# Performance work log

Measured on AMD Instinct MI355X. Metric: run time of the kernel, lower is better.

The kernel has to match this reference:

```python
import jax, jax.numpy as jnp
import numpy as np
from jax import lax

EPS = 1e-6
RADIUS = (5, 5, 5)          # box-filter window (must be odd for shape consistency)
GRADIENT_TYPE = "symmetric"  # {'active','passive','symmetric'}
SHAPE = (1, 1, 256, 256, 256)


def _box1d(x, axis, k):
    """Running-sum (integral image) 1D box filter of width k, 'same' padding floor(k/2)."""
    pad = (k - 1) // 2
    cfg = [(0, 0)] * x.ndim
    cfg[axis] = (pad, pad)
    xp = jnp.pad(x, cfg)
    c = jnp.cumsum(xp, axis=axis)
    cfg2 = [(0, 0)] * x.ndim
    cfg2[axis] = (1, 0)
    c = jnp.pad(c, cfg2)
    n = c.shape[axis]
    return lax.slice_in_dim(c, k, n, axis=axis) - lax.slice_in_dim(c, 0, n - k, axis=axis)


def _box3d(x):
    # separable uniform (all-ones) 3D box filter == F.conv3d with ones kernel
    for ax, k in zip((2, 3, 4), RADIUS):
        x = _box1d(x, ax, k)
    return x


def _grad1d(x, axis):
    """torch.gradient: central differences inside, one-sided at the edges, spacing=1."""
    n = x.shape[axis]
    central = (lax.slice_in_dim(x, 2, n, axis=axis) - lax.slice_in_dim(x, 0, n - 2, axis=axis)) * 0.5
    first = lax.slice_in_dim(x, 1, 2, axis=axis) - lax.slice_in_dim(x, 0, 1, axis=axis)
    last = lax.slice_in_dim(x, n - 1, n, axis=axis) - lax.slice_in_dim(x, n - 2, n - 1, axis=axis)
    return jnp.concatenate([first, central, last], axis=axis)


def _ncc_forces(image, reference_image):
    npix = float(np.prod(RADIUS))
    sum_i = _box3d(image)
    sum_r = _box3d(reference_image)
    sum_ii = _box3d(image * image)
    sum_rr = _box3d(reference_image * reference_image)
    sum_ir = _box3d(image * reference_image)

    image_mean = sum_i / npix
    reference_image_mean = sum_i / npix  # NOTE: faithful to original (uses sum_i, not sum_r)

    var_r = sum_rr - 2.0 * reference_image_mean * sum_r + npix * reference_image_mean * reference_image_mean
    var_i = sum_ii - 2.0 * image_mean * sum_i + npix * image_mean * image_mean
    cross = (sum_ir - reference_image_mean * sum_i - image_mean * sum_r
             + npix * image_mean * reference_image_mean)

    if GRADIENT_TYPE == "active":
        grads = [_grad1d(image, a) for a in (2, 3, 4)]
    elif GRADIENT_TYPE == "passive":
        grads = [_grad1d(reference_image, a) for a in (2, 3, 4)]
    elif GRADIENT_TYPE == "symmetric":
        grads = [0.5 * (_grad1d(image, a) + _grad1d(reference_image, a)) for a in (2, 3, 4)]
    else:
        raise ValueError("Unknown gradient type")

    factor = 2.0 * cross / (var_i * var_r + EPS) * (image - cross / var_r * reference_image)
    return -factor * jnp.concatenate(grads, axis=1)  # (B, 3, D, H, W)


def setup_inputs() -> dict:
    key = jax.random.key(0)
    k1, k2 = jax.random.split(key)
    return {
        "image": jax.random.normal(k1, SHAPE, dtype=jnp.float32),
        "mask": jnp.ones(SHAPE, dtype=jnp.float32),
        "reference_image": jax.random.normal(k2, SHAPE, dtype=jnp.float32),
        "reference_mask": jnp.ones(SHAPE, dtype=jnp.float32),
    }


def reference(image, mask, reference_image, reference_mask):
    # mask / reference_mask are accepted but unused, exactly as in the original module.
    return _ncc_forces(image, reference_image)
```

## Files before the change

### kernel.cpp

```cpp
#include <hip/hip_runtime.h>


#define DIM 256
#define TX  32
#define TY  8
#define ZCH 32
#define PXA 41
#define PY  12
#define NT  256
#define RS  5
#define YW  40
#define NF  5

#define LDS_BAR() asm volatile("s_waitcnt lgkmcnt(0)\n\ts_barrier" ::: "memory")

#define STEP(K, I, ISSUE, COMMIT) do {                                         \
    constexpr int sZ   = ((K) + 3) % RS;                                       \
    constexpr int sZP  = ((K) + 4) % RS;                                       \
    constexpr int sZM1 = ((K) + 2) % RS;                                       \
    constexpr int sZM2 = ((K) + 1) % RS;                                       \
    const int i_ = (I);                                                        \
         \
    if (pfAct) {                                                               \
        if (COMMIT) {                                                          \
            float* d_ = praw + (sZP * PY + prow) * PXA + pcol;                 \
            d_[0] = pf.x; d_[1] = pf.y; d_[2] = pf.z; d_[3] = pf.w;            \
        }                                                                      \
        if (ISSUE) {                                                           \
            float4 v_ = make_float4(0.f, 0.f, 0.f, 0.f);                       \
            if ((z0 + i_) < DIM && pxyOk)                                      \
                v_ = *(const float4*)pcur;                                     \
            pcur += (size_t)(DIM * DIM);                                       \
            pf = v_;                                                           \
        }                                                                      \
    }                                                                          \
    const int b_ = i_ & 1;                                                     \
            \
    if (bAct) {                                                                \
        float sA0=0.f,sA1=0.f,sB0=0.f,sB1=0.f,sAA0=0.f,sAA1=0.f;               \
        float sBB0=0.f,sBB1=0.f,sAB0=0.f,sAB1=0.f;                             \
        _Pragma("unroll")                                                      \
        for (int dy = 0; dy < 5; ++dy) {                                       \
            const float aI0 = rawI[sZ][brow + dy][bcol];                       \
            const float aI1 = rawI[sZ][brow + dy][bcol + 1];                   \
            const float aR0 = rawR[sZ][brow + dy][bcol];                       \
            const float aR1 = rawR[sZ][brow + dy][bcol + 1];                   \
            sA0 += aI0; sA1 += aI1; sB0 += aR0; sB1 += aR1;                    \
            sAA0 = fmaf(aI0, aI0, sAA0); sAA1 = fmaf(aI1, aI1, sAA1);          \
            sBB0 = fmaf(aR0, aR0, sBB0); sBB1 = fmaf(aR1, aR1, sBB1);          \
            sAB0 = fmaf(aI0, aR0, sAB0); sAB1 = fmaf(aI1, aR1, sAB1);          \
        }                                                                      \
        float* yp_ = &ytmp[b_][brow][bcol][0];                                 \
        yp_[0] = sA0; yp_[1] = sB0; yp_[2] = sAA0; yp_[3] = sBB0;              \
        yp_[4] = sAB0;                                                         \
        yp_[5] = sA1; yp_[6] = sB1; yp_[7] = sAA1; yp_[8] = sBB1;              \
        yp_[9] = sAB1;                                                         \
    }                                                                          \
    LDS_BAR();                                                                 \
         \
    float n_[NF];                                                              \
    {                                                                          \
        const float* yb_ = &ytmp[b_][ty][tx + 2][0];                           \
        _Pragma("unroll")                                                      \
        for (int f = 0; f < NF; ++f)                                           \
            n_[f] = yb_[f] + yb_[f+5] + yb_[f+10] + yb_[f+15] + yb_[f+20];     \
    }                                                                          \
                                 \
    cIm = cI0; cI0 = cIp; cIp = rawI[sZM1][ly][lx];                            \
    cRm = cR0; cR0 = cRp; cRp = rawR[sZM1][ly][lx];                            \
                                        \
    if (i_ >= 4) {                                                             \
        const int zc = z0 - 4 + i_;                                            \
        float zs[NF];                                                          \
        _Pragma("unroll")                                                      \
        for (int f = 0; f < NF; ++f)                                           \
            zs[f] = H[((K)+1)%RS][f] + H[((K)+2)%RS][f] + H[((K)+3)%RS][f]     \
                  + H[((K)+4)%RS][f] + n_[f];                                  \
        const float m     = zs[0] * (1.0f / 125.0f);                           \
        const float var_r = zs[3] - 2.0f * m * zs[1] + 125.0f * m * m;         \
        const float var_i = zs[2] - 2.0f * m * zs[0] + 125.0f * m * m;         \
        const float cross = zs[4] - m * zs[0] - m * zs[1] + 125.0f * m * m;    \
        float giz, grz;                                                        \
        if (zc == 0)            { giz = cIp - cI0; grz = cRp - cR0; }          \
        else if (zc == DIM - 1) { giz = cI0 - cIm; grz = cR0 - cRm; }          \
        else { giz = 0.5f * (cIp - cIm); grz = 0.5f * (cRp - cRm); }           \
        const float iyp = rawI[sZM2][ly + 1][lx], iym = rawI[sZM2][ly - 1][lx];\
        const float ryp = rawR[sZM2][ly + 1][lx], rym = rawR[sZM2][ly - 1][lx];\
        const float ixp = rawI[sZM2][ly][lx + 1], ixm = rawI[sZM2][ly][lx - 1];\
        const float rxp = rawR[sZM2][ly][lx + 1], rxm = rawR[sZM2][ly][lx - 1];\
        float giy, gry;                                                        \
        if (gy == 0)            { giy = iyp - cI0; gry = ryp - cR0; }          \
        else if (gy == DIM - 1) { giy = cI0 - iym; gry = cR0 - rym; }          \
        else { giy = 0.5f * (iyp - iym); gry = 0.5f * (ryp - rym); }           \
        float gix, grx;                                                        \
        if (gx == 0)            { gix = ixp - cI0; grx = rxp - cR0; }          \
        else if (gx == DIM - 1) { gix = cI0 - ixm; grx = cR0 - rxm; }          \
        else { gix = 0.5f * (ixp - ixm); grx = 0.5f * (rxp - rxm); }           \
        const float inv_d = __builtin_amdgcn_rcpf(fmaf(var_i, var_r, 1e-6f));  \
        const float inv_r = __builtin_amdgcn_rcpf(var_r);                      \
        const float factor = 2.0f * cross * inv_d * (cI0 - cross * inv_r * cR0);\
        const size_t CS    = (size_t)DIM * DIM * DIM;                          \
        const size_t base_ = ((size_t)zc * DIM + gy) * DIM + gx;               \
        __builtin_nontemporal_store(-factor * 0.5f * (giz + grz),              \
                                    &gOut[base_]);                             \
        __builtin_nontemporal_store(-factor * 0.5f * (giy + gry),              \
                                    &gOut[base_ + CS]);                        \
        __builtin_nontemporal_store(-factor * 0.5f * (gix + grx),              \
                                    &gOut[base_ + 2 * CS]);                    \
    }                                                                          \
                                 \
    _Pragma("unroll")                                                          \
    for (int f = 0; f < NF; ++f) H[(K)][f] = n_[f];                            \
} while (0)

__global__ __launch_bounds__(NT, 5) void ncc_forces_kernel(
    const float* __restrict__ gI,
    const float* __restrict__ gR,
    float* __restrict__ gOut)
{
    __shared__ float rawI[RS][PY][PXA];
    __shared__ float rawR[RS][PY][PXA];
    __shared__ float ytmp[2][TY][YW][NF];

    const int t  = threadIdx.x;
    const int tx = t & 31;
    const int ty = t >> 5;
    const int x0 = blockIdx.x * TX;
    const int y0 = blockIdx.y * TY;
    const int z0 = blockIdx.z * ZCH;

    const bool pfI   = (t < 120);
    const bool pfR   = (t >= 128 && t < 248);
    const bool pfAct = pfI || pfR;
    const int  pid   = pfI ? t : (t - 128);
    const int  prow  = pid / 10;
    const int  pcol  = (pid - prow * 10) * 4;
    const int  pgy   = y0 - 2 + prow;
    const int  pgx   = x0 - 4 + pcol;
    const float* pbase = pfI ? gI : gR;
    float*       praw  = pfI ? &rawI[0][0][0] : &rawR[0][0][0];
    const bool   pxyOk = ((unsigned)pgy < DIM) && ((unsigned)pgx < DIM);
    const size_t pgoff = pxyOk ? ((size_t)pgy * DIM + pgx) : 0;

    const bool bAct = (t < 144);
    const int  brow = t / 18;
    const int  bcol = 2 + (t - brow * 18) * 2;

    const int gy = y0 + ty;
    const int gx = x0 + tx;
    const int ly = ty + 2, lx = tx + 4;

    float4 pf = make_float4(0.f, 0.f, 0.f, 0.f);
    const float* pcur = pbase + (size_t)z0 * (DIM * DIM) + pgoff;

    float H[RS][NF];
    #pragma unroll
    for (int a = 0; a < RS; ++a)
        #pragma unroll
        for (int f = 0; f < NF; ++f) H[a][f] = 0.f;
    float cIm = 0.f, cI0 = 0.f, cIp = 0.f, cRm = 0.f, cR0 = 0.f, cRp = 0.f;

    if (pfAct) {
        float4 v = make_float4(0.f, 0.f, 0.f, 0.f);
        if ((z0 - 2) >= 0 && pxyOk)
            v = *(const float4*)(pbase + (size_t)(z0 - 2) * (DIM * DIM) + pgoff);
        float* d0 = praw + (3 * PY + prow) * PXA + pcol;
        d0[0] = v.x; d0[1] = v.y; d0[2] = v.z; d0[3] = v.w;
        float4 w = make_float4(0.f, 0.f, 0.f, 0.f);
        if ((z0 - 1) >= 0 && pxyOk)
            w = *(const float4*)(pbase + (size_t)(z0 - 1) * (DIM * DIM) + pgoff);
        pf = w;
    }
    LDS_BAR();

    #pragma clang loop unroll(disable)
    for (int ii = 0; ii < 30; ii += 5) {
        STEP(0, ii + 0, true, true);
        STEP(1, ii + 1, true, true);
        STEP(2, ii + 2, true, true);
        STEP(3, ii + 3, true, true);
        STEP(4, ii + 4, true, true);
    }
    STEP(0, 30, true,  true);
    STEP(1, 31, true,  true);
    STEP(2, 32, true,  true);
    STEP(3, 33, true,  true);
    STEP(4, 34, false, true);
    STEP(0, 35, false, false);
}

extern "C" void kernel_launch(void* const* d_in, const int* in_sizes, int n_in,
                              void* d_out, int out_size, void* d_ws, size_t ws_size,
                              hipStream_t stream) {
    const float* img = (const float*)d_in[0];
    const float* ref = (const float*)d_in[2];
    float* out = (float*)d_out;

    dim3 grid(DIM / TX, DIM / TY, DIM / ZCH);
    ncc_forces_kernel<<<grid, NT, 0, stream>>>(img, ref, out);
}
```

Before: 397.5 us.

## Interleave image and reference in shared memory as float2 for vector LDS access

Stores the image and reference tiles together in one interleaved float2 shared array instead of two separate float arrays. The box-filter x-pass can then read both values for two columns with a single float4 LDS load, and the gradient and center reads become float2 loads. Prefetch threads now load float2 from both inputs and commit a single float4 per step. Occupancy hint drops from 5 to 4 blocks, and LDS bank-conflict behaviour changes with the new 42-wide padded stride.

```diff
diff --git a/kernel.cpp b/kernel.cpp
--- a/kernel.cpp
+++ b/kernel.cpp
@@ -1,16 +1,16 @@
 #include <hip/hip_runtime.h>
 
 
-#define DIM 256
-#define TX  32
-#define TY  8
-#define ZCH 32
-#define PXA 41
-#define PY  12
-#define NT  256
-#define RS  5
-#define YW  40
-#define NF  5
+#define DIM  256
+#define TX   32
+#define TY   8
+#define ZCH  32
+#define PXA2 42
+#define PY   12
+#define NT   256
+#define RS   5
+#define YW   40
+#define NF   5
 
 #define LDS_BAR() asm volatile("s_waitcnt lgkmcnt(0)\n\ts_barrier" ::: "memory")
 
@@ -23,32 +23,33 @@
          \
     if (pfAct) {                                                               \
         if (COMMIT) {                                                          \
-            float* d_ = praw + (sZP * PY + prow) * PXA + pcol;                 \
-            d_[0] = pf.x; d_[1] = pf.y; d_[2] = pf.z; d_[3] = pf.w;            \
+            *(float4*)&rawIR[sZP][prow][pcell] =                               \
+                make_float4(pfi.x, pfr.x, pfi.y, pfr.y);                       \
         }                                                                      \
         if (ISSUE) {                                                           \
-            float4 v_ = make_float4(0.f, 0.f, 0.f, 0.f);                       \
-            if ((z0 + i_) < DIM && pxyOk)                                      \
-                v_ = *(const float4*)pcur;                                     \
-            pcur += (size_t)(DIM * DIM);                                       \
-            pf = v_;                                                           \
+            float2 vi = make_float2(0.f, 0.f), vr = make_float2(0.f, 0.f);     \
+            if ((z0 + i_) < DIM && pxyOk) {                                    \
+                vi = *(const float2*)pcurI;                                    \
+                vr = *(const float2*)pcurR;                                    \
+            }                                                                  \
+            pcurI += (size_t)(DIM * DIM);                                      \
+            pcurR += (size_t)(DIM * DIM);                                      \
+            pfi = vi; pfr = vr;                                                \
         }                                                                      \
     }                                                                          \
     const int b_ = i_ & 1;                                                     \
-            \
+        \
     if (bAct) {                                                                \
         float sA0=0.f,sA1=0.f,sB0=0.f,sB1=0.f,sAA0=0.f,sAA1=0.f;               \
         float sBB0=0.f,sBB1=0.f,sAB0=0.f,sAB1=0.f;                             \
         _Pragma("unroll")                                                      \
         for (int dy = 0; dy < 5; ++dy) {                                       \
-            const float aI0 = rawI[sZ][brow + dy][bcol];                       \
-            const float aI1 = rawI[sZ][brow + dy][bcol + 1];                   \
-            const float aR0 = rawR[sZ][brow + dy][bcol];                       \
-            const float aR1 = rawR[sZ][brow + dy][bcol + 1];                   \
-            sA0 += aI0; sA1 += aI1; sB0 += aR0; sB1 += aR1;                    \
-            sAA0 = fmaf(aI0, aI0, sAA0); sAA1 = fmaf(aI1, aI1, sAA1);          \
-            sBB0 = fmaf(aR0, aR0, sBB0); sBB1 = fmaf(aR1, aR1, sBB1);          \
-            sAB0 = fmaf(aI0, aR0, sAB0); sAB1 = fmaf(aI1, aR1, sAB1);          \
+            const float4 v = *(const float4*)&rawIR[sZ][brow + dy][bcol];      \
+            sA0 += v.x; sB0 += v.y; sA1 += v.z; sB1 += v.w;                    \
+            sAA0 = fmaf(v.x, v.x, sAA0); sBB0 = fmaf(v.y, v.y, sBB0);          \
+            sAB0 = fmaf(v.x, v.y, sAB0);                                       \
+            sAA1 = fmaf(v.z, v.z, sAA1); sBB1 = fmaf(v.w, v.w, sBB1);          \
+            sAB1 = fmaf(v.z, v.w, sAB1);                                       \
         }                                                                      \
         float* yp_ = &ytmp[b_][brow][bcol][0];                                 \
         yp_[0] = sA0; yp_[1] = sB0; yp_[2] = sAA0; yp_[3] = sBB0;              \
@@ -65,9 +66,12 @@
         for (int f = 0; f < NF; ++f)                                           \
             n_[f] = yb_[f] + yb_[f+5] + yb_[f+10] + yb_[f+15] + yb_[f+20];     \
     }                                                                          \
-                                 \
-    cIm = cI0; cI0 = cIp; cIp = rawI[sZM1][ly][lx];                            \
-    cRm = cR0; cR0 = cRp; cRp = rawR[sZM1][ly][lx];                            \
+                       \
+    {                                                                          \
+        const float2 c_ = rawIR[sZM1][ly][lx];                                 \
+        cIm = cI0; cI0 = cIp; cIp = c_.x;                                      \
+        cRm = cR0; cR0 = cRp; cRp = c_.y;                                      \
+    }                                                                          \
                                         \
     if (i_ >= 4) {                                                             \
         const int zc = z0 - 4 + i_;                                            \
@@ -84,18 +88,18 @@
         if (zc == 0)            { giz = cIp - cI0; grz = cRp - cR0; }          \
         else if (zc == DIM - 1) { giz = cI0 - cIm; grz = cR0 - cRm; }          \
         else { giz = 0.5f * (cIp - cIm); grz = 0.5f * (cRp - cRm); }           \
-        const float iyp = rawI[sZM2][ly + 1][lx], iym = rawI[sZM2][ly - 1][lx];\
-        const float ryp = rawR[sZM2][ly + 1][lx], rym = rawR[sZM2][ly - 1][lx];\
-        const float ixp = rawI[sZM2][ly][lx + 1], ixm = rawI[sZM2][ly][lx - 1];\
-        const float rxp = rawR[sZM2][ly][lx + 1], rxm = rawR[sZM2][ly][lx - 1];\
+        const float2 cyp = rawIR[sZM2][ly + 1][lx];                            \
+        const float2 cym = rawIR[sZM2][ly - 1][lx];                            \
+        const float2 cxp = rawIR[sZM2][ly][lx + 1];                            \
+        const float2 cxm = rawIR[sZM2][ly][lx - 1];                            \
         float giy, gry;                                                        \
-        if (gy == 0)            { giy = iyp - cI0; gry = ryp - cR0; }          \
-        else if (gy == DIM - 1) { giy = cI0 - iym; gry = cR0 - rym; }          \
-        else { giy = 0.5f * (iyp - iym); gry = 0.5f * (ryp - rym); }           \
+        if (gy == 0)            { giy = cyp.x - cI0; gry = cyp.y - cR0; }      \
+        else if (gy == DIM - 1) { giy = cI0 - cym.x; gry = cR0 - cym.y; }      \
+        else { giy = 0.5f * (cyp.x - cym.x); gry = 0.5f * (cyp.y - cym.y); }   \
         float gix, grx;                                                        \
-        if (gx == 0)            { gix = ixp - cI0; grx = rxp - cR0; }          \
-        else if (gx == DIM - 1) { gix = cI0 - ixm; grx = cR0 - rxm; }          \
-        else { gix = 0.5f * (ixp - ixm); grx = 0.5f * (rxp - rxm); }           \
+        if (gx == 0)            { gix = cxp.x - cI0; grx = cxp.y - cR0; }      \
+        else if (gx == DIM - 1) { gix = cI0 - cxm.x; grx = cR0 - cxm.y; }      \
+        else { gix = 0.5f * (cxp.x - cxm.x); grx = 0.5f * (cxp.y - cxm.y); }   \
         const float inv_d = __builtin_amdgcn_rcpf(fmaf(var_i, var_r, 1e-6f));  \
         const float inv_r = __builtin_amdgcn_rcpf(var_r);                      \
         const float factor = 2.0f * cross * inv_d * (cI0 - cross * inv_r * cR0);\
@@ -113,13 +117,12 @@
     for (int f = 0; f < NF; ++f) H[(K)][f] = n_[f];                            \
 } while (0)
 
-__global__ __launch_bounds__(NT, 5) void ncc_forces_kernel(
+__global__ __launch_bounds__(NT, 4) void ncc_forces_kernel(
     const float* __restrict__ gI,
     const float* __restrict__ gR,
     float* __restrict__ gOut)
 {
-    __shared__ float rawI[RS][PY][PXA];
-    __shared__ float rawR[RS][PY][PXA];
+    __shared__ __align__(16) float2 rawIR[RS][PY][PXA2];
     __shared__ float ytmp[2][TY][YW][NF];
 
     const int t  = threadIdx.x;
@@ -129,17 +132,12 @@
     const int y0 = blockIdx.y * TY;
     const int z0 = blockIdx.z * ZCH;
 
-    const bool pfI   = (t < 120);
-    const bool pfR   = (t >= 128 && t < 248);
-    const bool pfAct = pfI || pfR;
-    const int  pid   = pfI ? t : (t - 128);
-    const int  prow  = pid / 10;
-    const int  pcol  = (pid - prow * 10) * 4;
+    const bool pfAct = (t < 240);
+    const int  prow  = t / 20;
+    const int  pcell = (t - prow * 20) * 2;
     const int  pgy   = y0 - 2 + prow;
-    const int  pgx   = x0 - 4 + pcol;
-    const float* pbase = pfI ? gI : gR;
-    float*       praw  = pfI ? &rawI[0][0][0] : &rawR[0][0][0];
-    const bool   pxyOk = ((unsigned)pgy < DIM) && ((unsigned)pgx < DIM);
+    const int  pgx   = x0 - 4 + pcell;
+    const bool pxyOk = ((unsigned)pgy < DIM) && ((unsigned)pgx < DIM);
     const size_t pgoff = pxyOk ? ((size_t)pgy * DIM + pgx) : 0;
 
     const bool bAct = (t < 144);
@@ -150,8 +148,9 @@
     const int gx = x0 + tx;
     const int ly = ty + 2, lx = tx + 4;
 
-    float4 pf = make_float4(0.f, 0.f, 0.f, 0.f);
-    const float* pcur = pbase + (size_t)z0 * (DIM * DIM) + pgoff;
+    float2 pfi = make_float2(0.f, 0.f), pfr = make_float2(0.f, 0.f);
+    const float* pcurI = gI + (size_t)z0 * (DIM * DIM) + pgoff;
+    const float* pcurR = gR + (size_t)z0 * (DIM * DIM) + pgoff;
 
     float H[RS][NF];
     #pragma unroll
@@ -161,15 +160,18 @@
     float cIm = 0.f, cI0 = 0.f, cIp = 0.f, cRm = 0.f, cR0 = 0.f, cRp = 0.f;
 
     if (pfAct) {
-        float4 v = make_float4(0.f, 0.f, 0.f, 0.f);
-        if ((z0 - 2) >= 0 && pxyOk)
-            v = *(const float4*)(pbase + (size_t)(z0 - 2) * (DIM * DIM) + pgoff);
-        float* d0 = praw + (3 * PY + prow) * PXA + pcol;
-        d0[0] = v.x; d0[1] = v.y; d0[2] = v.z; d0[3] = v.w;
-        float4 w = make_float4(0.f, 0.f, 0.f, 0.f);
-        if ((z0 - 1) >= 0 && pxyOk)
-            w = *(const float4*)(pbase + (size_t)(z0 - 1) * (DIM * DIM) + pgoff);
-        pf = w;
+        float2 vi = make_float2(0.f, 0.f), vr = make_float2(0.f, 0.f);
+        if ((z0 - 2) >= 0 && pxyOk) {
+            vi = *(const float2*)(gI + (size_t)(z0 - 2) * (DIM * DIM) + pgoff);
+            vr = *(const float2*)(gR + (size_t)(z0 - 2) * (DIM * DIM) + pgoff);
+        }
+        *(float4*)&rawIR[3][prow][pcell] = make_float4(vi.x, vr.x, vi.y, vr.y);
+        float2 wi = make_float2(0.f, 0.f), wr = make_float2(0.f, 0.f);
+        if ((z0 - 1) >= 0 && pxyOk) {
+            wi = *(const float2*)(gI + (size_t)(z0 - 1) * (DIM * DIM) + pgoff);
+            wr = *(const float2*)(gR + (size_t)(z0 - 1) * (DIM * DIM) + pgoff);
+        }
+        pfi = wi; pfr = wr;
     }
     LDS_BAR();
 
```

Result: no change. 397.8 us (+0.1%).
